# Optimization experiments

Hardware: AMD Instinct MI355X
Metric: run time of the kernel (lower is better)

The kernel has to match this reference:

```python
import jax, jax.numpy as jnp
import numpy as np

# E2M1 FP4 code table: code = sign(1b) | magnitude(3b)
FP4_VALS = jnp.array([0.0, 0.5, 1.0, 1.5, 2.0, 3.0, 4.0, 6.0,
                      -0.0, -0.5, -1.0, -1.5, -2.0, -3.0, -4.0, -6.0], dtype=jnp.float32)
ALPHA = 1.702
LIMIT = 7.0
BLOCK = 32


def dequant_mxfp4(qw, scales):
    """qw: [N, K//2] byte values (two 4-bit codes, low nibble first);
    scales: [N, K//32] E8M0 exponents. Returns fp32 [N, K]."""
    lo = qw & 0xF
    hi = (qw >> 4) & 0xF
    codes = jnp.stack([lo, hi], axis=-1).reshape(qw.shape[0], -1)  # [N, K]
    w = FP4_VALS[codes]
    s = jnp.exp2((scales - 127).astype(jnp.float32))               # [N, K//32]
    N, K = w.shape
    w = w.reshape(N, K // BLOCK, BLOCK) * s[..., None]
    return w.reshape(N, K)


def setup_inputs() -> dict:
    key = jax.random.key(0)
    ks = jax.random.split(key, 9)
    T, H, I, E, TOPK = 1024, 2880, 2880, 8, 2
    return {
        "hidden_states": jax.random.normal(ks[0], (T, H), dtype=jnp.float32),
        "routing_weights": jax.random.uniform(ks[1], (T, TOPK), dtype=jnp.float32),
        "gate_up_proj_bias": jax.random.normal(ks[2], (E, 2 * I), dtype=jnp.float32),
        "down_proj_bias": jax.random.normal(ks[3], (E, H), dtype=jnp.float32),
        "router_indices": jax.random.randint(ks[4], (T, TOPK), 0, E, dtype=jnp.int32),
        "gate_up_qweight": jax.random.randint(ks[5], (E, 2 * I, H // 2), 0, 256, dtype=jnp.int32),
        "gate_up_scales": jax.random.randint(ks[6], (E, 2 * I, H // BLOCK), 118, 130, dtype=jnp.int32),
        "down_qweight": jax.random.randint(ks[7], (E, H, I // 2), 0, 256, dtype=jnp.int32),
        "down_scales": jax.random.randint(ks[8], (E, H, I // BLOCK), 118, 130, dtype=jnp.int32),
    }


def reference(hidden_states, routing_weights, gate_up_proj_bias, down_proj_bias,
              router_indices, gate_up_qweight, gate_up_scales, down_qweight, down_scales):
    E = gate_up_qweight.shape[0]
    out = jnp.zeros_like(hidden_states)
    for e in range(E):  # small fixed expert count
        # combined routing weight per token for expert e (0 if not routed);
        # equals the index_add over all top_k hits in the original loop
        w_e = jnp.sum(jnp.where(router_indices == e, routing_weights, 0.0), axis=-1)  # [T]
        wg = dequant_mxfp4(gate_up_qweight[e], gate_up_scales[e])  # [2I, H]
        gate_up = hidden_states @ wg.T + gate_up_proj_bias[e]      # [T, 2I]
        gate = jnp.minimum(gate_up[..., 0::2], LIMIT)
        up = jnp.clip(gate_up[..., 1::2], -LIMIT, LIMIT)
        glu = gate * jax.nn.sigmoid(gate * ALPHA)
        gated = (up + 1.0) * glu                                   # [T, I]
        wd = dequant_mxfp4(down_qweight[e], down_scales[e])        # [H, I]
        o = gated @ wd.T + down_proj_bias[e]                       # [T, H]
        out = out + o * w_e[:, None]
    return out
```

## Files before the change

### kernel.cpp

```cpp
#include <hip/hip_runtime.h>
#include <hip/hip_bf16.h>

typedef unsigned int uint;
typedef unsigned short ushort;
typedef __bf16 bf16x8 __attribute__((ext_vector_type(8)));
typedef float f32x4 __attribute__((ext_vector_type(4)));
typedef unsigned short u16x2 __attribute__((ext_vector_type(2)));

#define T_TOK 1024
#define HDIM 2880
#define IDIM 2880
#define NEXP 8
#define GU 5760
#define QK1 1440
#define SG1 90
#define QK2 1440
#define SG2 90
#define MAXR 2048
#define NK 45
#define BM 320

#define ZROW_OFF 65536u
#define HB_OFF 131072u
#define GATED_OFF_PRE 6029312u
#define WS_NEED (GATED_OFF_PRE + (size_t)MAXR * IDIM * 2)

static __device__ __forceinline__ int ls(int row, int c) {
  return (row << 6) + (((c ^ row) & 7) << 3);
}

static __device__ __forceinline__ uint pkadd16(uint a, uint b) {
  u16x2 x = __builtin_bit_cast(u16x2, a);
  u16x2 y = __builtin_bit_cast(u16x2, b);
  u16x2 r = x + y;
  return __builtin_bit_cast(uint, r);
}

static __device__ __forceinline__ void decode8(uint P, uint sAdd2, uint out[4]) {
  uint L  = P & 0x0F0F0F0Fu;
  uint Hh = (P >> 4) & 0x0F0F0F0Fu;
  uint Lm = L & 0x07070707u,  Hm = Hh & 0x07070707u;
  uint Lsg = (L & 0x08080808u) << 4, Hsg = (Hh & 0x08080808u) << 4;
  uint hiL = __builtin_amdgcn_perm(0x40404040u, 0x3F3F3F00u, Lm) | Lsg;
  uint hiH = __builtin_amdgcn_perm(0x40404040u, 0x3F3F3F00u, Hm) | Hsg;
  uint loL = __builtin_amdgcn_perm(0xC0804000u, 0xC0800000u, Lm);
  uint loH = __builtin_amdgcn_perm(0xC0804000u, 0xC0800000u, Hm);
  uint mL  = __builtin_amdgcn_perm(0xFFFFFFFFu, 0xFFFFFF00u, Lm);
  uint mH  = __builtin_amdgcn_perm(0xFFFFFFFFu, 0xFFFFFF00u, Hm);
  uint pL01 = __builtin_amdgcn_perm(hiL, loL, 0x05010400u);
  uint pL23 = __builtin_amdgcn_perm(hiL, loL, 0x07030602u);
  uint pH01 = __builtin_amdgcn_perm(hiH, loH, 0x05010400u);
  uint pH23 = __builtin_amdgcn_perm(hiH, loH, 0x07030602u);
  uint aL01 = pkadd16(pL01, sAdd2 & __builtin_amdgcn_perm(mL, mL, 0x01010000u));
  uint aL23 = pkadd16(pL23, sAdd2 & __builtin_amdgcn_perm(mL, mL, 0x03030202u));
  uint aH01 = pkadd16(pH01, sAdd2 & __builtin_amdgcn_perm(mH, mH, 0x01010000u));
  uint aH23 = pkadd16(pH23, sAdd2 & __builtin_amdgcn_perm(mH, mH, 0x03030202u));
  out[0] = __builtin_amdgcn_perm(aH01, aL01, 0x05040100u);
  out[1] = __builtin_amdgcn_perm(aH01, aL01, 0x07060302u);
  out[2] = __builtin_amdgcn_perm(aH23, aL23, 0x05040100u);
  out[3] = __builtin_amdgcn_perm(aH23, aL23, 0x07060302u);
}

static __device__ __forceinline__ uint packbf2(float a, float b) {
  ushort ua = __builtin_bit_cast(ushort, __float2bfloat16(a));
  ushort ub = __builtin_bit_cast(ushort, __float2bfloat16(b));
  return (uint)ua | ((uint)ub << 16);
}


__global__ void build_lists_kernel(const int* __restrict__ ridx,
                                   int* __restrict__ counts,
                                   int* __restrict__ lists) {
  int r = blockIdx.x * 256 + threadIdx.x;
  if (r >= MAXR) return;
  int e = ridx[r];
  int pos = atomicAdd(&counts[e], 1);
  lists[e * MAXR + pos] = r;
}


__global__ void cvt_kernel(const float* __restrict__ in, ushort* __restrict__ out) {
  int i = (blockIdx.x * 256 + threadIdx.x) * 8;
  float4 a = *(const float4*)(in + i);
  float4 b = *(const float4*)(in + i + 4);
  uint4 o;
  o.x = packbf2(a.x, a.y); o.y = packbf2(a.z, a.w);
  o.z = packbf2(b.x, b.y); o.w = packbf2(b.z, b.w);
  *(uint4*)(out + i) = o;
}


template <bool PRE>
__global__ __launch_bounds__(256, 3)
void gemm1_kernel(const char* __restrict__ wsb,
                  const float* __restrict__ hiddenF,
                  const int* __restrict__ guq,
                  const int* __restrict__ gus,
                  const float* __restrict__ gub,
                  const int* __restrict__ counts,
                  const int* __restrict__ lists,
                  ushort* __restrict__ gated) {
  const int e  = blockIdx.x & 7;
  const int xt = blockIdx.x >> 3;
  const int cnt = counts[e];
  const int mt = blockIdx.y;
  if (mt * BM >= cnt) return;
  const int gu0 = xt * 64;
  const int tid = threadIdx.x;

  __shared__ ushort lA[BM * 64];
  __shared__ ushort lB[64 * 64];
  __shared__ int rowid[BM];

  for (int i = tid; i < BM; i += 256) {
    int rl = mt * BM + i;
    rowid[i] = (rl < cnt) ? lists[e * MAXR + rl] : -1;
  }
  __syncthreads();

  const int ln = tid & 63, wv = tid >> 6;
  const int ln15 = ln & 15, kq = ln >> 4;

  uint aoff[10];
  uint avalid = 0;
  if (PRE) {
    #pragma unroll
    for (int j = 0; j < 10; ++j) {
      int slot = wv * 640 + j * 64 + ln;
      int row  = slot >> 3;
      int corig = (slot ^ row) & 7;
      int r = rowid[row];
      aoff[j] = (r >= 0) ? (HB_OFF + (uint)(r >> 1) * (HDIM * 2) + corig * 16)
                         : (ZROW_OFF + corig * 16);
    }
  } else {
    #pragma unroll
    for (int j = 0; j < 10; ++j) {
      int row = (tid >> 3) + 32 * j;
      int r = rowid[row];
      if (r >= 0) avalid |= 1u << j;
      uint tok = (r >= 0) ? (uint)(r >> 1) : 0u;
      aoff[j] = tok * (HDIM * 4) + (uint)(tid & 7) * 32;
    }
  }

  const int brow = tid >> 2, c2 = tid & 3;
  const uint grow = (uint)(e * GU + gu0 + brow);
  const uint boff0 = grow * (QK1 * 4) + (uint)c2 * 32;
  const uint soff0 = grow * (SG1 * 4) + (uint)(c2 >> 1) * 4;

  f32x4 acc[5][4];
  #pragma unroll
  for (int m = 0; m < 5; ++m)
    #pragma unroll
    for (int n = 0; n < 4; ++n) acc[m][n] = (f32x4)0.f;

  const char* gq = (const char*)guq;
  const char* gs = (const char*)gus;

  for (int ks = 0; ks < NK; ++ks) {
    int4 bv0 = *(const int4*)(gq + boff0 + (uint)ks * 128);
    int4 bv1 = *(const int4*)(gq + boff0 + (uint)ks * 128 + 16);
    int  sv  = *(const int*)(gs + soff0 + (uint)ks * 8);
    if (PRE) {
      #pragma unroll
      for (int j = 0; j < 10; ++j) {
        __builtin_amdgcn_global_load_lds(
            (const __attribute__((address_space(1))) void*)(wsb + aoff[j] + (uint)ks * 128),
            (__attribute__((address_space(3))) void*)((char*)lA + (wv * 640 + j * 64) * 16),
            16, 0, 0);
      }
    } else {
      #pragma unroll
      for (int j = 0; j < 10; ++j) {
        int row = (tid >> 3) + 32 * j;
        uint4 o;
        if (avalid & (1u << j)) {
          const float4* f = (const float4*)((const char*)hiddenF + aoff[j] + (size_t)ks * 256);
          float4 f0 = f[0], f1 = f[1];
          o.x = packbf2(f0.x, f0.y); o.y = packbf2(f0.z, f0.w);
          o.z = packbf2(f1.x, f1.y); o.w = packbf2(f1.z, f1.w);
        } else { o.x = o.y = o.z = o.w = 0u; }
        *(uint4*)&lA[ls(row, tid & 7)] = o;
      }
    }
    {
      uint P0 = (uint)bv0.x | ((uint)bv0.y << 8) | ((uint)bv0.z << 16) | ((uint)bv0.w << 24);
      uint P1 = (uint)bv1.x | ((uint)bv1.y << 8) | ((uint)bv1.z << 16) | ((uint)bv1.w << 24);
      uint sOff = ((uint)(sv - 127) << 7) & 0xFFFFu;
      uint sAdd2 = sOff | (sOff << 16);
      uint o0[4], o1[4];
      decode8(P0, sAdd2, o0);
      decode8(P1, sAdd2, o1);
      uint4 w0; w0.x = o0[0]; w0.y = o0[1]; w0.z = o0[2]; w0.w = o0[3];
      uint4 w1; w1.x = o1[0]; w1.y = o1[1]; w1.z = o1[2]; w1.w = o1[3];
      *(uint4*)&lB[ls(brow, 2 * c2)]     = w0;
      *(uint4*)&lB[ls(brow, 2 * c2 + 1)] = w1;
    }
    __syncthreads();
    __builtin_amdgcn_s_setprio(1);
    #pragma unroll
    for (int kf = 0; kf < 2; ++kf) {
      const int cc = 4 * kf + kq;
      bf16x8 bfr[4];
      #pragma unroll
      for (int n = 0; n < 4; ++n)
        bfr[n] = *(const bf16x8*)&lB[ls(n * 16 + ln15, cc)];
      #pragma unroll
      for (int m = 0; m < 5; ++m) {
        bf16x8 af = *(const bf16x8*)&lA[ls(wv * 80 + m * 16 + ln15, cc)];
        #pragma unroll
        for (int n = 0; n < 4; ++n)
          acc[m][n] = __builtin_amdgcn_mfma_f32_16x16x32_bf16(af, bfr[n], acc[m][n], 0, 0, 0);
      }
    }
    __builtin_amdgcn_s_setprio(0);
    __syncthreads();
  }

  float bias[4];
  #pragma unroll
  for (int n = 0; n < 4; ++n)
    bias[n] = gub[(size_t)e * GU + gu0 + n * 16 + ln15];
  #pragma unroll
  for (int m = 0; m < 5; ++m) {
    #pragma unroll
    for (int rg = 0; rg < 4; ++rg) {
      int row = wv * 80 + m * 16 + kq * 4 + rg;
      int r = rowid[row];
      #pragma unroll
      for (int n = 0; n < 4; ++n) {
        float x = acc[m][n][rg] + bias[n];
        float y = __shfl_xor(x, 1);
        if (r >= 0 && !(ln & 1)) {
          float g = fminf(x, 7.f);
          float u = fminf(fmaxf(y, -7.f), 7.f);
          float glu = g / (1.f + __expf(-1.702f * g));
          float val = (u + 1.f) * glu;
          int gucol = gu0 + n * 16 + ln15;
          gated[(size_t)r * IDIM + (gucol >> 1)] =
              __builtin_bit_cast(ushort, __float2bfloat16(val));
        }
      }
    }
  }
}


__global__ __launch_bounds__(256, 3)
void gemm2_kernel(const char* __restrict__ wsb, uint gatedOff,
                  const int* __restrict__ dq,
                  const int* __restrict__ dsc,
                  const float* __restrict__ dpb,
                  const float* __restrict__ routing,
                  const int* __restrict__ counts,
                  const int* __restrict__ lists,
                  float* __restrict__ outp) {
  const int e  = blockIdx.x & 7;
  const int ht = blockIdx.x >> 3;
  const int cnt = counts[e];
  const int mt = blockIdx.y;
  if (mt * BM >= cnt) return;
  const int h0 = ht * 32;
  const int tid = threadIdx.x;

  __shared__ ushort lA[BM * 64];
  __shared__ ushort lB[32 * 64];
  __shared__ int rowid[BM];

  for (int i = tid; i < BM; i += 256) {
    int rl = mt * BM + i;
    rowid[i] = (rl < cnt) ? lists[e * MAXR + rl] : -1;
  }
  __syncthreads();

  const int ln = tid & 63, wv = tid >> 6;
  const int ln15 = ln & 15, kq = ln >> 4;

  uint aoff[10];
  #pragma unroll
  for (int j = 0; j < 10; ++j) {
    int slot = wv * 640 + j * 64 + ln;
    int row  = slot >> 3;
    int corig = (slot ^ row) & 7;
    int r = rowid[row];
    aoff[j] = (r >= 0) ? (gatedOff + (uint)r * (IDIM * 2) + corig * 16)
                       : (ZROW_OFF + corig * 16);
  }
  const int brow = tid >> 2, c2 = tid & 3;
  const bool bact = (brow < 32);
  const uint hrow = (uint)(e * HDIM + h0 + (brow & 31));
  const uint boff0 = hrow * (QK2 * 4) + (uint)c2 * 32;
  const uint soff0 = hrow * (SG2 * 4) + (uint)(c2 >> 1) * 4;

  f32x4 acc[5][2];
  #pragma unroll
  for (int m = 0; m < 5; ++m) { acc[m][0] = (f32x4)0.f; acc[m][1] = (f32x4)0.f; }

  const char* gq = (const char*)dq;
  const char* gs = (const char*)dsc;

  for (int ks = 0; ks < NK; ++ks) {
    int4 bv0, bv1; int sv = 0;
    if (bact) {
      bv0 = *(const int4*)(gq + boff0 + (uint)ks * 128);
      bv1 = *(const int4*)(gq + boff0 + (uint)ks * 128 + 16);
      sv  = *(const int*)(gs + soff0 + (uint)ks * 8);
    }
    #pragma unroll
    for (int j = 0; j < 10; ++j) {
      __builtin_amdgcn_global_load_lds(
          (const __attribute__((address_space(1))) void*)(wsb + aoff[j] + (uint)ks * 128),
          (__attribute__((address_space(3))) void*)((char*)lA + (wv * 640 + j * 64) * 16),
          16, 0, 0);
    }
    if (bact) {
      uint P0 = (uint)bv0.x | ((uint)bv0.y << 8) | ((uint)bv0.z << 16) | ((uint)bv0.w << 24);
      uint P1 = (uint)bv1.x | ((uint)bv1.y << 8) | ((uint)bv1.z << 16) | ((uint)bv1.w << 24);
      uint sOff = ((uint)(sv - 127) << 7) & 0xFFFFu;
      uint sAdd2 = sOff | (sOff << 16);
      uint o0[4], o1[4];
      decode8(P0, sAdd2, o0);
      decode8(P1, sAdd2, o1);
      uint4 w0; w0.x = o0[0]; w0.y = o0[1]; w0.z = o0[2]; w0.w = o0[3];
      uint4 w1; w1.x = o1[0]; w1.y = o1[1]; w1.z = o1[2]; w1.w = o1[3];
      *(uint4*)&lB[ls(brow & 31, 2 * c2)]     = w0;
      *(uint4*)&lB[ls(brow & 31, 2 * c2 + 1)] = w1;
    }
    __syncthreads();
    __builtin_amdgcn_s_setprio(1);
    #pragma unroll
    for (int kf = 0; kf < 2; ++kf) {
      const int cc = 4 * kf + kq;
      bf16x8 bfr[2];
      #pragma unroll
      for (int n = 0; n < 2; ++n)
        bfr[n] = *(const bf16x8*)&lB[ls(n * 16 + ln15, cc)];
      #pragma unroll
      for (int m = 0; m < 5; ++m) {
        bf16x8 af = *(const bf16x8*)&lA[ls(wv * 80 + m * 16 + ln15, cc)];
        #pragma unroll
        for (int n = 0; n < 2; ++n)
          acc[m][n] = __builtin_amdgcn_mfma_f32_16x16x32_bf16(af, bfr[n], acc[m][n], 0, 0, 0);
      }
    }
    __builtin_amdgcn_s_setprio(0);
    __syncthreads();
  }

  float bias[2];
  #pragma unroll
  for (int n = 0; n < 2; ++n)
    bias[n] = dpb[(size_t)e * HDIM + h0 + n * 16 + ln15];
  #pragma unroll
  for (int m = 0; m < 5; ++m) {
    #pragma unroll
    for (int rg = 0; rg < 4; ++rg) {
      int row = wv * 80 + m * 16 + kq * 4 + rg;
      int r = rowid[row];
      if (r < 0) continue;
      float wgt = routing[r];
      #pragma unroll
      for (int n = 0; n < 2; ++n) {
        int hcol = h0 + n * 16 + ln15;
        atomicAdd(outp + (size_t)(r >> 1) * HDIM + hcol,
                  wgt * (acc[m][n][rg] + bias[n]));
      }
    }
  }
}


extern "C" void kernel_launch(void* const* d_in, const int* in_sizes, int n_in,
                              void* d_out, int out_size, void* d_ws, size_t ws_size,
                              hipStream_t stream) {
  const float* hidden  = (const float*)d_in[0];
  const float* routing = (const float*)d_in[1];
  const float* gub     = (const float*)d_in[2];
  const float* dpb     = (const float*)d_in[3];
  const int*   ridx    = (const int*)d_in[4];
  const int*   guq     = (const int*)d_in[5];
  const int*   gus     = (const int*)d_in[6];
  const int*   dq      = (const int*)d_in[7];
  const int*   dsc     = (const int*)d_in[8];
  float* outp = (float*)d_out;

  char* ws = (char*)d_ws;
  int* counts = (int*)ws;
  int* lists  = (int*)(ws + 256);
  const bool pre = (ws_size >= WS_NEED);
  const uint gatedOff = pre ? GATED_OFF_PRE : HB_OFF;
  ushort* hb    = (ushort*)(ws + HB_OFF);
  ushort* gated = (ushort*)(ws + gatedOff);

  hipMemsetAsync(counts, 0, 256, stream);
  hipMemsetAsync(ws + ZROW_OFF, 0, 5760, stream);
  hipMemsetAsync(d_out, 0, (size_t)out_size * sizeof(float), stream);

  build_lists_kernel<<<MAXR / 256, 256, 0, stream>>>(ridx, counts, lists);
  if (pre)
    cvt_kernel<<<(T_TOK * HDIM / 8) / 256, 256, 0, stream>>>(hidden, hb);

  dim3 grid1((GU / 64) * NEXP, (MAXR + BM - 1) / BM);
  if (pre)
    gemm1_kernel<true><<<grid1, 256, 0, stream>>>(ws, hidden, guq, gus, gub,
                                                  counts, lists, gated);
  else
    gemm1_kernel<false><<<grid1, 256, 0, stream>>>(ws, hidden, guq, gus, gub,
                                                   counts, lists, gated);

  dim3 grid2((HDIM / 32) * NEXP, (MAXR + BM - 1) / BM);
  gemm2_kernel<<<grid2, 256, 0, stream>>>(ws, gatedOff, dq, dsc, dpb, routing,
                                          counts, lists, outp);
}
```

Before: 289.7 us.

## Register-prefetch next K-step of A and B tiles, replacing direct-to-LDS loads

Both GEMM kernels now load the next K-step's activation rows and quantized weights into registers right after the barrier, so global loads overlap the MFMA work. The previous global_load_lds path and the zero-row scratch buffer are removed, and invalid rows are masked in registers instead. In gemm2 the weight decode is spread across all 256 threads instead of only the first 64 rows' worth. This raises register pressure (ten uint4 prefetch buffers) at launch bounds of 3 waves per SIMD, which may cause spills or lower occupancy.

```diff
diff --git a/kernel.cpp b/kernel.cpp
--- a/kernel.cpp
+++ b/kernel.cpp
@@ -20,7 +20,6 @@
 #define NK 45
 #define BM 320
 
-#define ZROW_OFF 65536u
 #define HB_OFF 131072u
 #define GATED_OFF_PRE 6029312u
 #define WS_NEED (GATED_OFF_PRE + (size_t)MAXR * IDIM * 2)
@@ -92,7 +91,7 @@
 
 template <bool PRE>
 __global__ __launch_bounds__(256, 3)
-void gemm1_kernel(const char* __restrict__ wsb,
+void gemm1_kernel(const ushort* __restrict__ hiddenB,
                   const float* __restrict__ hiddenF,
                   const int* __restrict__ guq,
                   const int* __restrict__ gus,
@@ -121,29 +120,17 @@
   const int ln = tid & 63, wv = tid >> 6;
   const int ln15 = ln & 15, kq = ln >> 4;
 
+  const int arow = tid >> 3, ac = tid & 7;
+  uint avalid = 0;
   uint aoff[10];
-  uint avalid = 0;
-  if (PRE) {
-    #pragma unroll
-    for (int j = 0; j < 10; ++j) {
-      int slot = wv * 640 + j * 64 + ln;
-      int row  = slot >> 3;
-      int corig = (slot ^ row) & 7;
-      int r = rowid[row];
-      aoff[j] = (r >= 0) ? (HB_OFF + (uint)(r >> 1) * (HDIM * 2) + corig * 16)
-                         : (ZROW_OFF + corig * 16);
-    }
-  } else {
-    #pragma unroll
-    for (int j = 0; j < 10; ++j) {
-      int row = (tid >> 3) + 32 * j;
-      int r = rowid[row];
-      if (r >= 0) avalid |= 1u << j;
-      uint tok = (r >= 0) ? (uint)(r >> 1) : 0u;
-      aoff[j] = tok * (HDIM * 4) + (uint)(tid & 7) * 32;
-    }
-  }
-
+  #pragma unroll
+  for (int j = 0; j < 10; ++j) {
+    int r = rowid[arow + 32 * j];
+    if (r >= 0) avalid |= 1u << j;
+    uint tok = (r >= 0) ? (uint)(r >> 1) : 0u;
+    aoff[j] = PRE ? (tok * (HDIM * 2) + (uint)ac * 16)
+                  : (tok * (HDIM * 4) + (uint)ac * 32);
+  }
   const int brow = tid >> 2, c2 = tid & 3;
   const uint grow = (uint)(e * GU + gu0 + brow);
   const uint boff0 = grow * (QK1 * 4) + (uint)c2 * 32;
@@ -157,33 +144,40 @@
 
   const char* gq = (const char*)guq;
   const char* gs = (const char*)gus;
+  const char* hB = (const char*)hiddenB;
+  const char* hF = (const char*)hiddenF;
+
+  uint4 aP[10];
+  int4  bv0, bv1;
+  int   sv;
+
+  auto load_step = [&](int ks) {
+    #pragma unroll
+    for (int j = 0; j < 10; ++j) {
+      if (avalid & (1u << j)) {
+        if (PRE) {
+          aP[j] = *(const uint4*)(hB + aoff[j] + (uint)ks * 128);
+        } else {
+          const float4* f = (const float4*)(hF + aoff[j] + (uint)ks * 256);
+          float4 f0 = f[0], f1 = f[1];
+          aP[j].x = packbf2(f0.x, f0.y); aP[j].y = packbf2(f0.z, f0.w);
+          aP[j].z = packbf2(f1.x, f1.y); aP[j].w = packbf2(f1.z, f1.w);
+        }
+      } else {
+        aP[j].x = aP[j].y = aP[j].z = aP[j].w = 0u;
+      }
+    }
+    bv0 = *(const int4*)(gq + boff0 + (uint)ks * 128);
+    bv1 = *(const int4*)(gq + boff0 + (uint)ks * 128 + 16);
+    sv  = *(const int*)(gs + soff0 + (uint)ks * 8);
+  };
+
+  load_step(0);
 
   for (int ks = 0; ks < NK; ++ks) {
-    int4 bv0 = *(const int4*)(gq + boff0 + (uint)ks * 128);
-    int4 bv1 = *(const int4*)(gq + boff0 + (uint)ks * 128 + 16);
-    int  sv  = *(const int*)(gs + soff0 + (uint)ks * 8);
-    if (PRE) {
-      #pragma unroll
-      for (int j = 0; j < 10; ++j) {
-        __builtin_amdgcn_global_load_lds(
-            (const __attribute__((address_space(1))) void*)(wsb + aoff[j] + (uint)ks * 128),
-            (__attribute__((address_space(3))) void*)((char*)lA + (wv * 640 + j * 64) * 16),
-            16, 0, 0);
-      }
-    } else {
-      #pragma unroll
-      for (int j = 0; j < 10; ++j) {
-        int row = (tid >> 3) + 32 * j;
-        uint4 o;
-        if (avalid & (1u << j)) {
-          const float4* f = (const float4*)((const char*)hiddenF + aoff[j] + (size_t)ks * 256);
-          float4 f0 = f[0], f1 = f[1];
-          o.x = packbf2(f0.x, f0.y); o.y = packbf2(f0.z, f0.w);
-          o.z = packbf2(f1.x, f1.y); o.w = packbf2(f1.z, f1.w);
-        } else { o.x = o.y = o.z = o.w = 0u; }
-        *(uint4*)&lA[ls(row, tid & 7)] = o;
-      }
-    }
+    #pragma unroll
+    for (int j = 0; j < 10; ++j)
+      *(uint4*)&lA[ls(arow + 32 * j, ac)] = aP[j];
     {
       uint P0 = (uint)bv0.x | ((uint)bv0.y << 8) | ((uint)bv0.z << 16) | ((uint)bv0.w << 24);
       uint P1 = (uint)bv1.x | ((uint)bv1.y << 8) | ((uint)bv1.z << 16) | ((uint)bv1.w << 24);
@@ -198,6 +192,7 @@
       *(uint4*)&lB[ls(brow, 2 * c2 + 1)] = w1;
     }
     __syncthreads();
+    if (ks + 1 < NK) load_step(ks + 1);
     __builtin_amdgcn_s_setprio(1);
     #pragma unroll
     for (int kf = 0; kf < 2; ++kf) {
@@ -248,7 +243,7 @@
 
 
 __global__ __launch_bounds__(256, 3)
-void gemm2_kernel(const char* __restrict__ wsb, uint gatedOff,
+void gemm2_kernel(const ushort* __restrict__ gated,
                   const int* __restrict__ dq,
                   const int* __restrict__ dsc,
                   const float* __restrict__ dpb,
@@ -277,21 +272,20 @@
   const int ln = tid & 63, wv = tid >> 6;
   const int ln15 = ln & 15, kq = ln >> 4;
 
+  const int arow = tid >> 3, ac = tid & 7;
+  uint avalid = 0;
   uint aoff[10];
   #pragma unroll
   for (int j = 0; j < 10; ++j) {
-    int slot = wv * 640 + j * 64 + ln;
-    int row  = slot >> 3;
-    int corig = (slot ^ row) & 7;
-    int r = rowid[row];
-    aoff[j] = (r >= 0) ? (gatedOff + (uint)r * (IDIM * 2) + corig * 16)
-                       : (ZROW_OFF + corig * 16);
-  }
-  const int brow = tid >> 2, c2 = tid & 3;
-  const bool bact = (brow < 32);
-  const uint hrow = (uint)(e * HDIM + h0 + (brow & 31));
-  const uint boff0 = hrow * (QK2 * 4) + (uint)c2 * 32;
-  const uint soff0 = hrow * (SG2 * 4) + (uint)(c2 >> 1) * 4;
+    int r = rowid[arow + 32 * j];
+    if (r >= 0) avalid |= 1u << j;
+    uint rr = (r >= 0) ? (uint)r : 0u;
+    aoff[j] = rr * (IDIM * 2) + (uint)ac * 16;
+  }
+  const int brow2 = tid >> 3, c3 = tid & 7;
+  const uint hrow = (uint)(e * HDIM + h0 + brow2);
+  const uint boff0 = hrow * (QK2 * 4) + (uint)c3 * 16;
+  const uint soff0 = hrow * (SG2 * 4) + (uint)(c3 >> 2) * 4;
 
   f32x4 acc[5][2];
   #pragma unroll
@@ -299,35 +293,39 @@
 
   const char* gq = (const char*)dq;
   const char* gs = (const char*)dsc;
+  const char* gA = (const char*)gated;
+
+  uint4 aP[10];
+  int4  bv;
+  int   sv;
+
+  auto load_step = [&](int ks) {
+    #pragma unroll
+    for (int j = 0; j < 10; ++j) {
+      if (avalid & (1u << j)) aP[j] = *(const uint4*)(gA + aoff[j] + (uint)ks * 128);
+      else { aP[j].x = aP[j].y = aP[j].z = aP[j].w = 0u; }
+    }
+    bv = *(const int4*)(gq + boff0 + (uint)ks * 128);
+    sv = *(const int*)(gs + soff0 + (uint)ks * 8);
+  };
+
+  load_step(0);
 
   for (int ks = 0; ks < NK; ++ks) {
-    int4 bv0, bv1; int sv = 0;
-    if (bact) {
-      bv0 = *(const int4*)(gq + boff0 + (uint)ks * 128);
-      bv1 = *(const int4*)(gq + boff0 + (uint)ks * 128 + 16);
-      sv  = *(const int*)(gs + soff0 + (uint)ks * 8);
-    }
-    #pragma unroll
-    for (int j = 0; j < 10; ++j) {
-      __builtin_amdgcn_global_load_lds(
-          (const __attribute__((address_space(1))) void*)(wsb + aoff[j] + (uint)ks * 128),
-          (__attribute__((address_space(3))) void*)((char*)lA + (wv * 640 + j * 64) * 16),
-          16, 0, 0);
-    }
-    if (bact) {
-      uint P0 = (uint)bv0.x | ((uint)bv0.y << 8) | ((uint)bv0.z << 16) | ((uint)bv0.w << 24);
-      uint P1 = (uint)bv1.x | ((uint)bv1.y << 8) | ((uint)bv1.z << 16) | ((uint)bv1.w << 24);
+    #pragma unroll
+    for (int j = 0; j < 10; ++j)
+      *(uint4*)&lA[ls(arow + 32 * j, ac)] = aP[j];
+    {
+      uint P = (uint)bv.x | ((uint)bv.y << 8) | ((uint)bv.z << 16) | ((uint)bv.w << 24);
       uint sOff = ((uint)(sv - 127) << 7) & 0xFFFFu;
       uint sAdd2 = sOff | (sOff << 16);
-      uint o0[4], o1[4];
-      decode8(P0, sAdd2, o0);
-      decode8(P1, sAdd2, o1);
-      uint4 w0; w0.x = o0[0]; w0.y = o0[1]; w0.z = o0[2]; w0.w = o0[3];
-      uint4 w1; w1.x = o1[0]; w1.y = o1[1]; w1.z = o1[2]; w1.w = o1[3];
-      *(uint4*)&lB[ls(brow & 31, 2 * c2)]     = w0;
-      *(uint4*)&lB[ls(brow & 31, 2 * c2 + 1)] = w1;
+      uint o[4];
+      decode8(P, sAdd2, o);
+      uint4 w; w.x = o[0]; w.y = o[1]; w.z = o[2]; w.w = o[3];
+      *(uint4*)&lB[ls(brow2, c3)] = w;
     }
     __syncthreads();
+    if (ks + 1 < NK) load_step(ks + 1);
     __builtin_amdgcn_s_setprio(1);
     #pragma unroll
     for (int kf = 0; kf < 2; ++kf) {
@@ -394,7 +392,6 @@
   ushort* gated = (ushort*)(ws + gatedOff);
 
   hipMemsetAsync(counts, 0, 256, stream);
-  hipMemsetAsync(ws + ZROW_OFF, 0, 5760, stream);
   hipMemsetAsync(d_out, 0, (size_t)out_size * sizeof(float), stream);
 
   build_lists_kernel<<<MAXR / 256, 256, 0, stream>>>(ridx, counts, lists);
@@ -403,13 +400,13 @@
 
   dim3 grid1((GU / 64) * NEXP, (MAXR + BM - 1) / BM);
   if (pre)
-    gemm1_kernel<true><<<grid1, 256, 0, stream>>>(ws, hidden, guq, gus, gub,
+    gemm1_kernel<true><<<grid1, 256, 0, stream>>>(hb, hidden, guq, gus, gub,
                                                   counts, lists, gated);
   else
-    gemm1_kernel<false><<<grid1, 256, 0, stream>>>(ws, hidden, guq, gus, gub,
+    gemm1_kernel<false><<<grid1, 256, 0, stream>>>(hb, hidden, guq, gus, gub,
                                                    counts, lists, gated);
 
   dim3 grid2((HDIM / 32) * NEXP, (MAXR + BM - 1) / BM);
-  gemm2_kernel<<<grid2, 256, 0, stream>>>(ws, gatedOff, dq, dsc, dpb, routing,
+  gemm2_kernel<<<grid2, 256, 0, stream>>>(gated, dq, dsc, dpb, routing,
                                           counts, lists, outp);
 }
```

Measured after the change: 356.8 us. +23.2%, slower.

## Double-buffer loads and widen MoE GEMM tiles to 512-thread blocks

Applied to the files above, without the earlier changes.

Both GEMM kernels move to 512-thread blocks laid out as a 4x2 wave grid, doubling the N tile (128 gate_up columns, 64 down columns) so each dequantized weight tile is shared by more waves. The K loop is restructured as a software pipeline. Weight loads are prefetched two steps ahead into alternating registers, and the A-tile global-to-LDS DMA for the next step is issued right after the compute barrier. Explicit waitcnt and sched_barrier fences control the ordering. The non-precomputed path is split into a separate fallback kernel, and the zero-row scratch is moved and enlarged. The risks are higher register pressure, fewer resident blocks per CU, and possible correctness hazards from the hand-written waitcnt counts.

```diff
diff --git a/kernel.cpp b/kernel.cpp
--- a/kernel.cpp
+++ b/kernel.cpp
@@ -20,7 +20,7 @@
 #define NK 45
 #define BM 320
 
-#define ZROW_OFF 65536u
+#define ZROW_OFF 98304u
 #define HB_OFF 131072u
 #define GATED_OFF_PRE 6029312u
 #define WS_NEED (GATED_OFF_PRE + (size_t)MAXR * IDIM * 2)
@@ -67,6 +67,9 @@
   return (uint)ua | ((uint)ub << 16);
 }
 
+#define SFENCE() __builtin_amdgcn_sched_barrier(0)
+#define SBAR() do { SFENCE(); __builtin_amdgcn_s_barrier(); SFENCE(); } while (0)
+
 
 __global__ void build_lists_kernel(const int* __restrict__ ridx,
                                    int* __restrict__ counts,
@@ -90,10 +93,8 @@
 }
 
 
-template <bool PRE>
-__global__ __launch_bounds__(256, 3)
+__global__ __launch_bounds__(512, 4)
 void gemm1_kernel(const char* __restrict__ wsb,
-                  const float* __restrict__ hiddenF,
                   const int* __restrict__ guq,
                   const int* __restrict__ gus,
                   const float* __restrict__ gub,
@@ -105,14 +106,14 @@
   const int cnt = counts[e];
   const int mt = blockIdx.y;
   if (mt * BM >= cnt) return;
-  const int gu0 = xt * 64;
+  const int gu0 = xt * 128;
   const int tid = threadIdx.x;
 
   __shared__ ushort lA[BM * 64];
-  __shared__ ushort lB[64 * 64];
+  __shared__ ushort lB[128 * 64];
   __shared__ int rowid[BM];
 
-  for (int i = tid; i < BM; i += 256) {
+  for (int i = tid; i < BM; i += 512) {
     int rl = mt * BM + i;
     rowid[i] = (rl < cnt) ? lists[e * MAXR + rl] : -1;
   }
@@ -120,73 +121,59 @@
 
   const int ln = tid & 63, wv = tid >> 6;
   const int ln15 = ln & 15, kq = ln >> 4;
-
-  uint aoff[10];
-  uint avalid = 0;
-  if (PRE) {
-    #pragma unroll
-    for (int j = 0; j < 10; ++j) {
-      int slot = wv * 640 + j * 64 + ln;
-      int row  = slot >> 3;
-      int corig = (slot ^ row) & 7;
-      int r = rowid[row];
-      aoff[j] = (r >= 0) ? (HB_OFF + (uint)(r >> 1) * (HDIM * 2) + corig * 16)
-                         : (ZROW_OFF + corig * 16);
-    }
-  } else {
-    #pragma unroll
-    for (int j = 0; j < 10; ++j) {
-      int row = (tid >> 3) + 32 * j;
-      int r = rowid[row];
-      if (r >= 0) avalid |= 1u << j;
-      uint tok = (r >= 0) ? (uint)(r >> 1) : 0u;
-      aoff[j] = tok * (HDIM * 4) + (uint)(tid & 7) * 32;
-    }
-  }
-
+  const int wm = wv & 3, wn = wv >> 2;
+
+  uint aoff[5];
+  #pragma unroll
+  for (int j = 0; j < 5; ++j) {
+    int slot = wv * 320 + j * 64 + ln;
+    int row  = slot >> 3;
+    int corig = (slot ^ row) & 7;
+    int r = rowid[row];
+    aoff[j] = (r >= 0) ? (HB_OFF + (uint)(r >> 1) * (HDIM * 2) + corig * 16)
+                       : (ZROW_OFF + corig * 16);
+  }
   const int brow = tid >> 2, c2 = tid & 3;
   const uint grow = (uint)(e * GU + gu0 + brow);
   const uint boff0 = grow * (QK1 * 4) + (uint)c2 * 32;
   const uint soff0 = grow * (SG1 * 4) + (uint)(c2 >> 1) * 4;
-
-  f32x4 acc[5][4];
-  #pragma unroll
-  for (int m = 0; m < 5; ++m)
-    #pragma unroll
-    for (int n = 0; n < 4; ++n) acc[m][n] = (f32x4)0.f;
-
   const char* gq = (const char*)guq;
   const char* gs = (const char*)gus;
 
-  for (int ks = 0; ks < NK; ++ks) {
-    int4 bv0 = *(const int4*)(gq + boff0 + (uint)ks * 128);
-    int4 bv1 = *(const int4*)(gq + boff0 + (uint)ks * 128 + 16);
-    int  sv  = *(const int*)(gs + soff0 + (uint)ks * 8);
-    if (PRE) {
-      #pragma unroll
-      for (int j = 0; j < 10; ++j) {
-        __builtin_amdgcn_global_load_lds(
-            (const __attribute__((address_space(1))) void*)(wsb + aoff[j] + (uint)ks * 128),
-            (__attribute__((address_space(3))) void*)((char*)lA + (wv * 640 + j * 64) * 16),
-            16, 0, 0);
-      }
-    } else {
-      #pragma unroll
-      for (int j = 0; j < 10; ++j) {
-        int row = (tid >> 3) + 32 * j;
-        uint4 o;
-        if (avalid & (1u << j)) {
-          const float4* f = (const float4*)((const char*)hiddenF + aoff[j] + (size_t)ks * 256);
-          float4 f0 = f[0], f1 = f[1];
-          o.x = packbf2(f0.x, f0.y); o.y = packbf2(f0.z, f0.w);
-          o.z = packbf2(f1.x, f1.y); o.w = packbf2(f1.z, f1.w);
-        } else { o.x = o.y = o.z = o.w = 0u; }
-        *(uint4*)&lA[ls(row, tid & 7)] = o;
-      }
-    }
+  f32x4 acc[5][4];
+  #pragma unroll
+  for (int m = 0; m < 5; ++m)
+    #pragma unroll
+    for (int n = 0; n < 4; ++n) acc[m][n] = (f32x4)0.f;
+
+  int4 qa0, qa1, qb0, qb1;
+  int  sa, sb;
+
+  auto dmaA = [&](int ka) {
+    #pragma unroll
+    for (int j = 0; j < 5; ++j)
+      __builtin_amdgcn_global_load_lds(
+          (const __attribute__((address_space(1))) void*)(wsb + aoff[j] + (uint)ka * 128),
+          (__attribute__((address_space(3))) void*)((char*)lA + (wv * 320 + j * 64) * 16),
+          16, 0, 0);
+  };
+  auto loadB = [&](int kb, int4& q0, int4& q1, int& sv) {
+    q0 = *(const int4*)(gq + boff0 + (uint)kb * 128);
+    q1 = *(const int4*)(gq + boff0 + (uint)kb * 128 + 16);
+    sv = *(const int*)(gs + soff0 + (uint)kb * 8);
+  };
+
+  loadB(0, qa0, qa1, sa);
+  SFENCE();
+  dmaA(0);
+  SFENCE();
+  loadB(1, qb0, qb1, sb);
+  SFENCE();
+
+  auto step = [&](int ks, int4& q0, int4& q1, int& sv) {
     {
-      uint P0 = (uint)bv0.x | ((uint)bv0.y << 8) | ((uint)bv0.z << 16) | ((uint)bv0.w << 24);
-      uint P1 = (uint)bv1.x | ((uint)bv1.y << 8) | ((uint)bv1.z << 16) | ((uint)bv1.w << 24);
+      uint P0 = (uint)q0.x | ((uint)q0.y << 8) | ((uint)q0.z << 16) | ((uint)q0.w << 24);
+      uint P1 = (uint)q1.x | ((uint)q1.y << 8) | ((uint)q1.z << 16) | ((uint)q1.w << 24);
       uint sOff = ((uint)(sv - 127) << 7) & 0xFFFFu;
       uint sAdd2 = sOff | (sOff << 16);
       uint o0[4], o1[4];
@@ -197,11 +184,149 @@
       *(uint4*)&lB[ls(brow, 2 * c2)]     = w0;
       *(uint4*)&lB[ls(brow, 2 * c2 + 1)] = w1;
     }
+    SFENCE();
+    asm volatile("s_waitcnt vmcnt(3) lgkmcnt(0)" ::: "memory");
+    SBAR();
+    __builtin_amdgcn_s_setprio(1);
+    #pragma unroll
+    for (int kf = 0; kf < 2; ++kf) {
+      const int cc = kf * 4 + kq;
+      bf16x8 b0 = *(const bf16x8*)&lB[ls(wn * 64 +  0 + ln15, cc)];
+      bf16x8 b1 = *(const bf16x8*)&lB[ls(wn * 64 + 16 + ln15, cc)];
+      bf16x8 b2 = *(const bf16x8*)&lB[ls(wn * 64 + 32 + ln15, cc)];
+      bf16x8 b3 = *(const bf16x8*)&lB[ls(wn * 64 + 48 + ln15, cc)];
+      #pragma unroll
+      for (int m = 0; m < 5; ++m) {
+        bf16x8 af = *(const bf16x8*)&lA[ls(wm * 80 + m * 16 + ln15, cc)];
+        acc[m][0] = __builtin_amdgcn_mfma_f32_16x16x32_bf16(af, b0, acc[m][0], 0, 0, 0);
+        acc[m][1] = __builtin_amdgcn_mfma_f32_16x16x32_bf16(af, b1, acc[m][1], 0, 0, 0);
+        acc[m][2] = __builtin_amdgcn_mfma_f32_16x16x32_bf16(af, b2, acc[m][2], 0, 0, 0);
+        acc[m][3] = __builtin_amdgcn_mfma_f32_16x16x32_bf16(af, b3, acc[m][3], 0, 0, 0);
+      }
+    }
+    __builtin_amdgcn_s_setprio(0);
+    SBAR();
+    dmaA((ks + 1 < NK) ? ks + 1 : NK - 1);
+    SFENCE();
+    {
+      int kb = (ks + 2 < NK) ? ks + 2 : NK - 1;
+      loadB(kb, q0, q1, sv);
+    }
+    SFENCE();
+  };
+
+  for (int ks = 0; ks < NK - 1; ks += 2) {
+    step(ks,     qa0, qa1, sa);
+    step(ks + 1, qb0, qb1, sb);
+  }
+  step(NK - 1, qa0, qa1, sa);
+  asm volatile("s_waitcnt vmcnt(0)" ::: "memory");
+
+  float bias[4];
+  #pragma unroll
+  for (int n = 0; n < 4; ++n)
+    bias[n] = gub[(size_t)e * GU + gu0 + wn * 64 + n * 16 + ln15];
+  #pragma unroll
+  for (int m = 0; m < 5; ++m) {
+    #pragma unroll
+    for (int rg = 0; rg < 4; ++rg) {
+      int row = wm * 80 + m * 16 + kq * 4 + rg;
+      int r = rowid[row];
+      #pragma unroll
+      for (int n = 0; n < 4; ++n) {
+        float x = acc[m][n][rg] + bias[n];
+        float y = __shfl_xor(x, 1);
+        if (r >= 0 && !(ln & 1)) {
+          float g = fminf(x, 7.f);
+          float u = fminf(fmaxf(y, -7.f), 7.f);
+          float glu = g / (1.f + __expf(-1.702f * g));
+          float val = (u + 1.f) * glu;
+          int gucol = gu0 + wn * 64 + n * 16 + ln15;
+          gated[(size_t)r * IDIM + (gucol >> 1)] =
+              __builtin_bit_cast(ushort, __float2bfloat16(val));
+        }
+      }
+    }
+  }
+}
+
+
+__global__ __launch_bounds__(256, 2)
+void gemm1_fb(const float* __restrict__ hiddenF,
+              const int* __restrict__ guq,
+              const int* __restrict__ gus,
+              const float* __restrict__ gub,
+              const int* __restrict__ counts,
+              const int* __restrict__ lists,
+              ushort* __restrict__ gated) {
+  const int e  = blockIdx.x & 7;
+  const int xt = blockIdx.x >> 3;
+  const int cnt = counts[e];
+  const int mt = blockIdx.y;
+  if (mt * BM >= cnt) return;
+  const int gu0 = xt * 64;
+  const int tid = threadIdx.x;
+
+  __shared__ ushort lA[BM * 64];
+  __shared__ ushort lB[64 * 64];
+  __shared__ int rowid[BM];
+
+  for (int i = tid; i < BM; i += 256) {
+    int rl = mt * BM + i;
+    rowid[i] = (rl < cnt) ? lists[e * MAXR + rl] : -1;
+  }
+  __syncthreads();
+
+  const int ln = tid & 63, wv = tid >> 6;
+  const int ln15 = ln & 15, kq = ln >> 4;
+  const int arow = tid >> 3, ac = tid & 7;
+  const int brow = tid >> 2, c2 = tid & 3;
+  const uint grow = (uint)(e * GU + gu0 + brow);
+  const uint boff0 = grow * (QK1 * 4) + (uint)c2 * 32;
+  const uint soff0 = grow * (SG1 * 4) + (uint)(c2 >> 1) * 4;
+  const char* gq = (const char*)guq;
+  const char* gs = (const char*)gus;
+
+  f32x4 acc[5][4];
+  #pragma unroll
+  for (int m = 0; m < 5; ++m)
+    #pragma unroll
+    for (int n = 0; n < 4; ++n) acc[m][n] = (f32x4)0.f;
+
+  for (int ks = 0; ks < NK; ++ks) {
+    #pragma unroll
+    for (int j = 0; j < 10; ++j) {
+      int row = arow + 32 * j;
+      int r = rowid[row];
+      uint4 o;
+      if (r >= 0) {
+        const float4* f = (const float4*)(hiddenF + (size_t)(r >> 1) * HDIM + ac * 8 + ks * 64);
+        float4 f0 = f[0], f1 = f[1];
+        o.x = packbf2(f0.x, f0.y); o.y = packbf2(f0.z, f0.w);
+        o.z = packbf2(f1.x, f1.y); o.w = packbf2(f1.z, f1.w);
+      } else { o.x = o.y = o.z = o.w = 0u; }
+      *(uint4*)&lA[ls(row, ac)] = o;
+    }
+    {
+      int4 b0 = *(const int4*)(gq + boff0 + (uint)ks * 128);
+      int4 b1 = *(const int4*)(gq + boff0 + (uint)ks * 128 + 16);
+      int  sv = *(const int*)(gs + soff0 + (uint)ks * 8);
+      uint P0 = (uint)b0.x | ((uint)b0.y << 8) | ((uint)b0.z << 16) | ((uint)b0.w << 24);
+      uint P1 = (uint)b1.x | ((uint)b1.y << 8) | ((uint)b1.z << 16) | ((uint)b1.w << 24);
+      uint sOff = ((uint)(sv - 127) << 7) & 0xFFFFu;
+      uint sAdd2 = sOff | (sOff << 16);
+      uint o0[4], o1[4];
+      decode8(P0, sAdd2, o0);
+      decode8(P1, sAdd2, o1);
+      uint4 w0; w0.x = o0[0]; w0.y = o0[1]; w0.z = o0[2]; w0.w = o0[3];
+      uint4 w1; w1.x = o1[0]; w1.y = o1[1]; w1.z = o1[2]; w1.w = o1[3];
+      *(uint4*)&lB[ls(brow, 2 * c2)]     = w0;
+      *(uint4*)&lB[ls(brow, 2 * c2 + 1)] = w1;
+    }
     __syncthreads();
-    __builtin_amdgcn_s_setprio(1);
     #pragma unroll
     for (int kf = 0; kf < 2; ++kf) {
-      const int cc = 4 * kf + kq;
+      const int cc = kf * 4 + kq;
       bf16x8 bfr[4];
       #pragma unroll
       for (int n = 0; n < 4; ++n)
@@ -214,7 +339,6 @@
           acc[m][n] = __builtin_amdgcn_mfma_f32_16x16x32_bf16(af, bfr[n], acc[m][n], 0, 0, 0);
       }
     }
-    __builtin_amdgcn_s_setprio(0);
     __syncthreads();
   }
 
@@ -247,7 +371,7 @@
 }
 
 
-__global__ __launch_bounds__(256, 3)
+__global__ __launch_bounds__(512, 4)
 void gemm2_kernel(const char* __restrict__ wsb, uint gatedOff,
                   const int* __restrict__ dq,
                   const int* __restrict__ dsc,
@@ -261,14 +385,14 @@
   const int cnt = counts[e];
   const int mt = blockIdx.y;
   if (mt * BM >= cnt) return;
-  const int h0 = ht * 32;
+  const int h0 = ht * 64;
   const int tid = threadIdx.x;
 
   __shared__ ushort lA[BM * 64];
-  __shared__ ushort lB[32 * 64];
+  __shared__ ushort lB[64 * 64];
   __shared__ int rowid[BM];
 
-  for (int i = tid; i < BM; i += 256) {
+  for (int i = tid; i < BM; i += 512) {
     int rl = mt * BM + i;
     rowid[i] = (rl < cnt) ? lists[e * MAXR + rl] : -1;
   }
@@ -276,93 +400,108 @@
 
   const int ln = tid & 63, wv = tid >> 6;
   const int ln15 = ln & 15, kq = ln >> 4;
-
-  uint aoff[10];
-  #pragma unroll
-  for (int j = 0; j < 10; ++j) {
-    int slot = wv * 640 + j * 64 + ln;
+  const int wm = wv & 3, wn = wv >> 2;
+
+  uint aoff[5];
+  #pragma unroll
+  for (int j = 0; j < 5; ++j) {
+    int slot = wv * 320 + j * 64 + ln;
     int row  = slot >> 3;
     int corig = (slot ^ row) & 7;
     int r = rowid[row];
     aoff[j] = (r >= 0) ? (gatedOff + (uint)r * (IDIM * 2) + corig * 16)
                        : (ZROW_OFF + corig * 16);
   }
-  const int brow = tid >> 2, c2 = tid & 3;
-  const bool bact = (brow < 32);
-  const uint hrow = (uint)(e * HDIM + h0 + (brow & 31));
-  const uint boff0 = hrow * (QK2 * 4) + (uint)c2 * 32;
-  const uint soff0 = hrow * (SG2 * 4) + (uint)(c2 >> 1) * 4;
-
-  f32x4 acc[5][2];
-  #pragma unroll
-  for (int m = 0; m < 5; ++m) { acc[m][0] = (f32x4)0.f; acc[m][1] = (f32x4)0.f; }
-
+  const int brow = tid >> 3, c3 = tid & 7;
+  const uint hrow = (uint)(e * HDIM + h0 + brow);
+  const uint boff0 = hrow * (QK2 * 4) + (uint)c3 * 16;
+  const uint soff0 = hrow * (SG2 * 4) + (uint)(c3 >> 2) * 4;
   const char* gq = (const char*)dq;
   const char* gs = (const char*)dsc;
 
-  for (int ks = 0; ks < NK; ++ks) {
-    int4 bv0, bv1; int sv = 0;
-    if (bact) {
-      bv0 = *(const int4*)(gq + boff0 + (uint)ks * 128);
-      bv1 = *(const int4*)(gq + boff0 + (uint)ks * 128 + 16);
-      sv  = *(const int*)(gs + soff0 + (uint)ks * 8);
-    }
-    #pragma unroll
-    for (int j = 0; j < 10; ++j) {
+  f32x4 acc[5][2];
+  #pragma unroll
+  for (int m = 0; m < 5; ++m) { acc[m][0] = (f32x4)0.f; acc[m][1] = (f32x4)0.f; }
+
+  int4 qa; int sa;
+  int4 qb; int sb;
+
+  auto dmaA = [&](int ka) {
+    #pragma unroll
+    for (int j = 0; j < 5; ++j)
       __builtin_amdgcn_global_load_lds(
-          (const __attribute__((address_space(1))) void*)(wsb + aoff[j] + (uint)ks * 128),
-          (__attribute__((address_space(3))) void*)((char*)lA + (wv * 640 + j * 64) * 16),
+          (const __attribute__((address_space(1))) void*)(wsb + aoff[j] + (uint)ka * 128),
+          (__attribute__((address_space(3))) void*)((char*)lA + (wv * 320 + j * 64) * 16),
           16, 0, 0);
-    }
-    if (bact) {
-      uint P0 = (uint)bv0.x | ((uint)bv0.y << 8) | ((uint)bv0.z << 16) | ((uint)bv0.w << 24);
-      uint P1 = (uint)bv1.x | ((uint)bv1.y << 8) | ((uint)bv1.z << 16) | ((uint)bv1.w << 24);
+  };
+  auto loadB = [&](int kb, int4& q0, int& sv) {
+    q0 = *(const int4*)(gq + boff0 + (uint)kb * 128);
+    sv = *(const int*)(gs + soff0 + (uint)kb * 8);
+  };
+
+  loadB(0, qa, sa);
+  SFENCE();
+  dmaA(0);
+  SFENCE();
+  loadB(1, qb, sb);
+  SFENCE();
+
+  auto step = [&](int ks, int4& q0, int& sv) {
+    {
+      uint P = (uint)q0.x | ((uint)q0.y << 8) | ((uint)q0.z << 16) | ((uint)q0.w << 24);
       uint sOff = ((uint)(sv - 127) << 7) & 0xFFFFu;
       uint sAdd2 = sOff | (sOff << 16);
-      uint o0[4], o1[4];
-      decode8(P0, sAdd2, o0);
-      decode8(P1, sAdd2, o1);
-      uint4 w0; w0.x = o0[0]; w0.y = o0[1]; w0.z = o0[2]; w0.w = o0[3];
-      uint4 w1; w1.x = o1[0]; w1.y = o1[1]; w1.z = o1[2]; w1.w = o1[3];
-      *(uint4*)&lB[ls(brow & 31, 2 * c2)]     = w0;
-      *(uint4*)&lB[ls(brow & 31, 2 * c2 + 1)] = w1;
-    }
-    __syncthreads();
+      uint o[4];
+      decode8(P, sAdd2, o);
+      uint4 w; w.x = o[0]; w.y = o[1]; w.z = o[2]; w.w = o[3];
+      *(uint4*)&lB[ls(brow, c3)] = w;
+    }
+    SFENCE();
+    asm volatile("s_waitcnt vmcnt(2) lgkmcnt(0)" ::: "memory");
+    SBAR();
     __builtin_amdgcn_s_setprio(1);
     #pragma unroll
     for (int kf = 0; kf < 2; ++kf) {
-      const int cc = 4 * kf + kq;
-      bf16x8 bfr[2];
-      #pragma unroll
-      for (int n = 0; n < 2; ++n)
-        bfr[n] = *(const bf16x8*)&lB[ls(n * 16 + ln15, cc)];
+      const int cc = kf * 4 + kq;
+      bf16x8 b0 = *(const bf16x8*)&lB[ls(wn * 32 +  0 + ln15, cc)];
+      bf16x8 b1 = *(const bf16x8*)&lB[ls(wn * 32 + 16 + ln15, cc)];
       #pragma unroll
       for (int m = 0; m < 5; ++m) {
-        bf16x8 af = *(const bf16x8*)&lA[ls(wv * 80 + m * 16 + ln15, cc)];
-        #pragma unroll
-        for (int n = 0; n < 2; ++n)
-          acc[m][n] = __builtin_amdgcn_mfma_f32_16x16x32_bf16(af, bfr[n], acc[m][n], 0, 0, 0);
+        bf16x8 af = *(const bf16x8*)&lA[ls(wm * 80 + m * 16 + ln15, cc)];
+        acc[m][0] = __builtin_amdgcn_mfma_f32_16x16x32_bf16(af, b0, acc[m][0], 0, 0, 0);
+        acc[m][1] = __builtin_amdgcn_mfma_f32_16x16x32_bf16(af, b1, acc[m][1], 0, 0, 0);
       }
     }
     __builtin_amdgcn_s_setprio(0);
-    __syncthreads();
-  }
+    SBAR();
+    dmaA((ks + 1 < NK) ? ks + 1 : NK - 1);
+    SFENCE();
+    loadB((ks + 2 < NK) ? ks + 2 : NK - 1, q0, sv);
+    SFENCE();
+  };
+
+  for (int ks = 0; ks < NK - 1; ks += 2) {
+    step(ks,     qa, sa);
+    step(ks + 1, qb, sb);
+  }
+  step(NK - 1, qa, sa);
+  asm volatile("s_waitcnt vmcnt(0)" ::: "memory");
 
   float bias[2];
   #pragma unroll
   for (int n = 0; n < 2; ++n)
-    bias[n] = dpb[(size_t)e * HDIM + h0 + n * 16 + ln15];
+    bias[n] = dpb[(size_t)e * HDIM + h0 + wn * 32 + n * 16 + ln15];
   #pragma unroll
   for (int m = 0; m < 5; ++m) {
     #pragma unroll
     for (int rg = 0; rg < 4; ++rg) {
-      int row = wv * 80 + m * 16 + kq * 4 + rg;
+      int row = wm * 80 + m * 16 + kq * 4 + rg;
       int r = rowid[row];
       if (r < 0) continue;
       float wgt = routing[r];
       #pragma unroll
       for (int n = 0; n < 2; ++n) {
-        int hcol = h0 + n * 16 + ln15;
+        int hcol = h0 + wn * 32 + n * 16 + ln15;
         atomicAdd(outp + (size_t)(r >> 1) * HDIM + hcol,
                   wgt * (acc[m][n][rg] + bias[n]));
       }
@@ -394,22 +533,23 @@
   ushort* gated = (ushort*)(ws + gatedOff);
 
   hipMemsetAsync(counts, 0, 256, stream);
-  hipMemsetAsync(ws + ZROW_OFF, 0, 5760, stream);
+  hipMemsetAsync(ws + ZROW_OFF, 0, 8192, stream);
   hipMemsetAsync(d_out, 0, (size_t)out_size * sizeof(float), stream);
 
   build_lists_kernel<<<MAXR / 256, 256, 0, stream>>>(ridx, counts, lists);
   if (pre)
     cvt_kernel<<<(T_TOK * HDIM / 8) / 256, 256, 0, stream>>>(hidden, hb);
 
-  dim3 grid1((GU / 64) * NEXP, (MAXR + BM - 1) / BM);
-  if (pre)
-    gemm1_kernel<true><<<grid1, 256, 0, stream>>>(ws, hidden, guq, gus, gub,
-                                                  counts, lists, gated);
-  else
-    gemm1_kernel<false><<<grid1, 256, 0, stream>>>(ws, hidden, guq, gus, gub,
-                                                   counts, lists, gated);
-
-  dim3 grid2((HDIM / 32) * NEXP, (MAXR + BM - 1) / BM);
-  gemm2_kernel<<<grid2, 256, 0, stream>>>(ws, gatedOff, dq, dsc, dpb, routing,
+  const int mtiles = (MAXR + BM - 1) / BM;
+  if (pre) {
+    dim3 grid1((GU / 128) * NEXP, mtiles);
+    gemm1_kernel<<<grid1, 512, 0, stream>>>(ws, guq, gus, gub, counts, lists, gated);
+  } else {
+    dim3 grid1f((GU / 64) * NEXP, mtiles);
+    gemm1_fb<<<grid1f, 256, 0, stream>>>(hidden, guq, gus, gub, counts, lists, gated);
+  }
+
+  dim3 grid2((HDIM / 64) * NEXP, mtiles);
+  gemm2_kernel<<<grid2, 512, 0, stream>>>(ws, gatedOff, dq, dsc, dpb, routing,
                                           counts, lists, outp);
 }
```

After: 696.5 us. 2.4x slower.
